# Kernel optimization log

Measured on AMD Instinct MI355X. Metric: run time of the kernel, lower is better.

The kernel has to match this reference:

```python
import jax, jax.numpy as jnp
import numpy as np

NEMB = 128
N_NODES = 8192
N_EDGES = 16384
N_STEMS = 4096
N_GRAPHS = 256
N_BLOCKS = 105       # BlockDictionary.n_unique_blocks
N_STEMTYPES = 32     # BlockDictionary.n_stem_types
OUT_PER_STEM = 105
OUT_PER_STOP = 1
NUM_CONV_STEPS = 12
SLOPE = 0.01         # nn.LeakyReLU default negative slope


def _act(v):
    return jax.nn.leaky_relu(v, SLOPE)


def setup_inputs() -> dict:
    key = jax.random.key(0)
    ks = jax.random.split(key, 32)
    def p(i, shape, fan_in):
        return jax.random.normal(ks[i], shape, jnp.float32) / np.sqrt(fan_in).astype(np.float32)
    D = NEMB
    inp = {
        "x": jax.random.randint(ks[0], (N_NODES,), 0, N_BLOCKS + 1),
        "stemtypes": jax.random.randint(ks[1], (N_STEMS,), 0, N_STEMTYPES + 1),
        "edge_attr": jax.random.randint(ks[2], (N_EDGES, 2), 0, N_STEMTYPES),
        "edge_index": jax.random.randint(ks[3], (2, N_EDGES), 0, N_NODES),
        "stem_node_idx": jax.random.randint(ks[4], (N_STEMS,), 0, N_NODES),
        "node_batch": jnp.sort(jax.random.randint(ks[5], (N_NODES,), 0, N_GRAPHS)),
        # embedding tables
        "emb_block": p(6, (N_BLOCKS + 1, D), D),
        "emb_stem": p(7, (N_STEMTYPES + 1, D), D),
        "emb_bond": p(8, (N_STEMTYPES, D), D),
        # block2emb MLP
        "b2e_w1": p(9, (D, D), D), "b2e_b1": p(10, (D,), D),
        "b2e_w2": p(11, (D, D), D), "b2e_b2": p(12, (D,), D),
        # NNConv root weight + bias (edge-nn is identity: nn.Sequential())
        "conv_root": p(13, (D, D), D), "conv_bias": p(14, (D,), D),
        # GRU (torch gate order r, z, n)
        "gru_w_ih": p(15, (3 * D, D), D), "gru_w_hh": p(16, (3 * D, D), D),
        "gru_b_ih": p(17, (3 * D,), D), "gru_b_hh": p(18, (3 * D,), D),
        # stem2pred MLP (in = 2*D)
        "s2p_w1": p(19, (D, 2 * D), 2 * D), "s2p_b1": p(20, (D,), 2 * D),
        "s2p_w2": p(21, (D, D), D), "s2p_b2": p(22, (D,), D),
        "s2p_w3": p(23, (OUT_PER_STEM, D), D), "s2p_b3": p(24, (OUT_PER_STEM,), D),
        # global2pred MLP
        "g2p_w1": p(25, (D, D), D), "g2p_b1": p(26, (D,), D),
        "g2p_w2": p(27, (OUT_PER_STOP, D), D), "g2p_b2": p(28, (OUT_PER_STOP,), D),
    }
    return inp


def reference(x, stemtypes, edge_attr, edge_index, stem_node_idx, node_batch,
              emb_block, emb_stem, emb_bond,
              b2e_w1, b2e_b1, b2e_w2, b2e_b2,
              conv_root, conv_bias,
              gru_w_ih, gru_w_hh, gru_b_ih, gru_b_hh,
              s2p_w1, s2p_b1, s2p_w2, s2p_b2, s2p_w3, s2p_b3,
              g2p_w1, g2p_b1, g2p_w2, g2p_b2):
    block_emb = emb_block[x]                          # [N, D]
    stem_emb = emb_stem[stemtypes]                    # [S, D]
    be = emb_bond[edge_attr]                          # [E, 2, D]
    # outer product -> per-edge [D_in, D_out] weight (matches view(-1, in, out))
    W_e = be[:, 0, :, None] * be[:, 1, None, :]       # [E, D, D]

    out = _act(block_emb @ b2e_w1.T + b2e_b1) @ b2e_w2.T + b2e_b2  # [N, D]
    h = out                                           # GRU hidden state

    src, dst = edge_index[0], edge_index[1]
    ones_e = jnp.ones((N_EDGES,), out.dtype)
    deg = jax.ops.segment_sum(ones_e, dst, num_segments=N_NODES)
    inv_deg = jnp.where(deg > 0, 1.0 / jnp.maximum(deg, 1.0), 0.0)[:, None]

    for _ in range(NUM_CONV_STEPS):
        # NNConv: mean_j (x_j @ W_e) + x @ root + bias, then LeakyReLU
        msg = jnp.einsum('ei,eij->ej', out[src], W_e)                  # [E, D]
        agg = jax.ops.segment_sum(msg, dst, num_segments=N_NODES) * inv_deg
        m = _act(agg + out @ conv_root + conv_bias)
        # single-layer GRU, seq_len = 1
        gi = m @ gru_w_ih.T + gru_b_ih
        gh = h @ gru_w_hh.T + gru_b_hh
        ir, iz, inn = jnp.split(gi, 3, axis=-1)
        hr, hz, hn = jnp.split(gh, 3, axis=-1)
        r = jax.nn.sigmoid(ir + hr)
        z = jax.nn.sigmoid(iz + hz)
        n = jnp.tanh(inn + r * hn)
        h = (1.0 - z) * n + z * h
        out = h

    stem_cat = jnp.concatenate([out[stem_node_idx], stem_emb], axis=1)  # [S, 2D]
    s = _act(stem_cat @ s2p_w1.T + s2p_b1)
    s = _act(s @ s2p_w2.T + s2p_b2)
    stem_pred = s @ s2p_w3.T + s2p_b3                                   # [S, out_per_stem]

    # global_mean_pool
    gsum = jax.ops.segment_sum(out, node_batch, num_segments=N_GRAPHS)
    gcnt = jax.ops.segment_sum(jnp.ones((N_NODES,), out.dtype), node_batch, num_segments=N_GRAPHS)
    gmean = gsum / jnp.maximum(gcnt, 1.0)[:, None]
    g = _act(gmean @ g2p_w1.T + g2p_b1)
    stop_pred = g @ g2p_w2.T + g2p_b2                                   # [G, out_per_stop]
    return stem_pred, stop_pred
```

## Files before the change

kernel.cpp:

```cpp
#include <hip/hip_runtime.h>
#include <math.h>

#define D 128
#define NNODES 8192
#define NEDGES 16384
#define NSTEMS 4096
#define NGRAPHS 256
#define NSTEPS 12
#define OPS 105
#define SLOPE 0.01f
#define MT 32
#define NB (NNODES / MT)
#define LDA 136
#define LDA2 264
#define LDQ 40
#define LDH 132

typedef _Float16 half_t;
typedef __attribute__((ext_vector_type(8))) _Float16 f16x8;
typedef __attribute__((ext_vector_type(4))) float f32x4;

__device__ __forceinline__ float leaky(float x) { return x > 0.f ? x : SLOPE * x; }
__device__ __forceinline__ float fast_sigmoid(float x) {
    return __builtin_amdgcn_rcpf(1.f + __expf(-x));
}
__device__ __forceinline__ float fast_tanh(float x) {
    float e = __expf(2.f * x);
    return 1.f - 2.f * __builtin_amdgcn_rcpf(e + 1.f);
}

__global__ void k_setup(
    const float* __restrict__ root, const float* __restrict__ wih,
    const float* __restrict__ whh, const float* __restrict__ bond,
    const float* __restrict__ sw1, const float* __restrict__ sw2,
    const float* __restrict__ sw3, const float* __restrict__ bw1,
    const float* __restrict__ bw2, const float* __restrict__ gw1,
    half_t* __restrict__ rootP, half_t* __restrict__ WihP,
    half_t* __restrict__ WhhP, half_t* __restrict__ bondTP,
    half_t* __restrict__ s1P, half_t* __restrict__ s2P, half_t* __restrict__ s3P,
    half_t* __restrict__ w1P, half_t* __restrict__ w2P, half_t* __restrict__ bondQP,
    float* __restrict__ g1T, int* __restrict__ zeroi) {
    int idx = blockIdx.x * 256 + threadIdx.x;
    int which = blockIdx.y;
    if (which == 10) {
        if (idx < 128 * 128) {
            int r = idx >> 7, c = idx & 127;
            g1T[c * 128 + r] = gw1[idx];
        }
        return;
    }
    if (which == 11) {
        if (idx < 2 * NNODES) zeroi[idx] = 0;
        return;
    }
    int KT = (which == 4) ? 8 : (which == 9) ? 1 : 4;
    int NT = (which == 1 || which == 2) ? 24 : (which == 3) ? 2 : (which == 6) ? 7 : 8;
    if (idx >= NT * KT * 512) return;
    int j = idx & 7;
    int L = (idx >> 3) & 63;
    int t = idx >> 9;
    int kt = t % KT, nt = t / KT;
    int k = kt * 32 + (L >> 4) * 8 + j;
    int n = nt * 16 + (L & 15);
    switch (which) {
        case 0: rootP[idx] = (half_t)root[k * D + n]; break;
        case 1: WihP[idx] = (half_t)wih[n * D + k]; break;
        case 2: WhhP[idx] = (half_t)whh[n * D + k]; break;
        case 3: bondTP[idx] = (half_t)bond[n * D + k]; break;
        case 4: s1P[idx] = (half_t)sw1[n * 256 + k]; break;
        case 5: s2P[idx] = (half_t)sw2[n * 128 + k]; break;
        case 6: s3P[idx] = (n < OPS) ? (half_t)sw3[n * 128 + k] : (half_t)0.f; break;
        case 7: w1P[idx] = (half_t)bw1[n * D + k]; break;
        case 8: w2P[idx] = (half_t)bw2[n * D + k]; break;
        case 9: bondQP[idx] = (half_t)bond[k * D + n]; break;
    }
}

__global__ void k_deg(const int* __restrict__ eidx, int* __restrict__ deg) {
    int e = blockIdx.x * 256 + threadIdx.x;
    if (e < NEDGES) atomicAdd(&deg[eidx[NEDGES + e]], 1);
}

__global__ void k_scan(const int* __restrict__ deg, int* __restrict__ row_start,
                       float* __restrict__ inv_deg) {
    __shared__ int sums[256];
    int t = threadIdx.x;
    int base = t * 32;
    int s = 0;
    for (int k = 0; k < 32; ++k) s += deg[base + k];
    sums[t] = s;
    __syncthreads();
    for (int off = 1; off < 256; off <<= 1) {
        int v = sums[t];
        int u = (t >= off) ? sums[t - off] : 0;
        __syncthreads();
        sums[t] = v + u;
        __syncthreads();
    }
    int run = sums[t] - s;
    for (int k = 0; k < 32; ++k) {
        int d = deg[base + k];
        row_start[base + k] = run;
        run += d;
        inv_deg[base + k] = (d > 0) ? (1.0f / (float)d) : 0.0f;
    }
    if (t == 255) row_start[NNODES] = run;
}

__global__ void k_scatter(const int* __restrict__ eidx, const int* __restrict__ eattr,
                          const int* __restrict__ row_start,
                          int* __restrict__ fill, int4* __restrict__ epack) {
    int e = blockIdx.x * 256 + threadIdx.x;
    if (e < NEDGES) {
        int d = eidx[NEDGES + e];
        int pos = row_start[d] + atomicAdd(&fill[d], 1);
        int2 aa = *(const int2*)(eattr + 2 * e);
        epack[pos] = make_int4(eidx[e], aa.x, aa.y, d);
    }
}

__global__ __launch_bounds__(512, 2) void k_init(
    const int* __restrict__ x, const float* __restrict__ embBlock,
    const half_t* __restrict__ w1P, const float* __restrict__ b1,
    const half_t* __restrict__ w2P, const float* __restrict__ b2,
    const half_t* __restrict__ bondTP,
    float* __restrict__ hF, float* __restrict__ P0) {
    __shared__ __align__(16) half_t Ae[MT * LDA];
    __shared__ __align__(16) half_t T1[MT * LDA];
    const int tid = threadIdx.x;
    const int w = tid >> 6;
    const int lane = tid & 63;
    const int quad = lane >> 4;
    const int l16 = lane & 15;
    const int n0 = blockIdx.x * MT;
    const int c = w * 16 + l16;

    {
        int row = tid >> 4;
        int col = (tid & 15) * 8;
        const float* src = embBlock + (size_t)x[n0 + row] * D + col;
        float4 v0 = ((const float4*)src)[0];
        float4 v1 = ((const float4*)src)[1];
        f16x8 hv;
        hv[0] = (half_t)v0.x; hv[1] = (half_t)v0.y; hv[2] = (half_t)v0.z; hv[3] = (half_t)v0.w;
        hv[4] = (half_t)v1.x; hv[5] = (half_t)v1.y; hv[6] = (half_t)v1.z; hv[7] = (half_t)v1.w;
        *(f16x8*)&Ae[row * LDA + col] = hv;
    }
    __syncthreads();

    {
        f32x4 acc[2] = {{0.f, 0.f, 0.f, 0.f}, {0.f, 0.f, 0.f, 0.f}};
#pragma unroll
        for (int kt = 0; kt < 4; ++kt) {
            f16x8 b = *(const f16x8*)(w1P + (size_t)((w * 4 + kt) * 64 + lane) * 8);
            f16x8 a0 = *(const f16x8*)&Ae[(0 + l16) * LDA + kt * 32 + quad * 8];
            f16x8 a1 = *(const f16x8*)&Ae[(16 + l16) * LDA + kt * 32 + quad * 8];
            acc[0] = __builtin_amdgcn_mfma_f32_16x16x32_f16(a0, b, acc[0], 0, 0, 0);
            acc[1] = __builtin_amdgcn_mfma_f32_16x16x32_f16(a1, b, acc[1], 0, 0, 0);
        }
        float bb = b1[c];
#pragma unroll
        for (int mt = 0; mt < 2; ++mt)
#pragma unroll
            for (int r = 0; r < 4; ++r)
                T1[(mt * 16 + quad * 4 + r) * LDA + c] = (half_t)leaky(acc[mt][r] + bb);
    }
    __syncthreads();

    {
        f32x4 acc[2] = {{0.f, 0.f, 0.f, 0.f}, {0.f, 0.f, 0.f, 0.f}};
#pragma unroll
        for (int kt = 0; kt < 4; ++kt) {
            f16x8 b = *(const f16x8*)(w2P + (size_t)((w * 4 + kt) * 64 + lane) * 8);
            f16x8 a0 = *(const f16x8*)&T1[(0 + l16) * LDA + kt * 32 + quad * 8];
            f16x8 a1 = *(const f16x8*)&T1[(16 + l16) * LDA + kt * 32 + quad * 8];
            acc[0] = __builtin_amdgcn_mfma_f32_16x16x32_f16(a0, b, acc[0], 0, 0, 0);
            acc[1] = __builtin_amdgcn_mfma_f32_16x16x32_f16(a1, b, acc[1], 0, 0, 0);
        }
        float bb = b2[c];
#pragma unroll
        for (int mt = 0; mt < 2; ++mt)
#pragma unroll
            for (int r = 0; r < 4; ++r) {
                int row = mt * 16 + quad * 4 + r;
                float h = acc[mt][r] + bb;
                hF[(size_t)(n0 + row) * D + c] = h;
                Ae[row * LDA + c] = (half_t)h;
            }
    }
    __syncthreads();

    if (w < 4) {
        int mt = w >> 1, nt = w & 1;
        f32x4 acc = {0.f, 0.f, 0.f, 0.f};
#pragma unroll
        for (int kt = 0; kt < 4; ++kt) {
            f16x8 b = *(const f16x8*)(bondTP + (size_t)((nt * 4 + kt) * 64 + lane) * 8);
            f16x8 a = *(const f16x8*)&Ae[(mt * 16 + l16) * LDA + kt * 32 + quad * 8];
            acc = __builtin_amdgcn_mfma_f32_16x16x32_f16(a, b, acc, 0, 0, 0);
        }
#pragma unroll
        for (int r = 0; r < 4; ++r)
            P0[(size_t)(n0 + mt * 16 + quad * 4 + r) * 32 + nt * 16 + l16] = acc[r];
    }
}

__global__ __launch_bounds__(512, 2) void k_step(
    float* __restrict__ hF,
    const float* __restrict__ Pprev, float* __restrict__ Pnext,
    const half_t* __restrict__ rootP, const half_t* __restrict__ WihP,
    const half_t* __restrict__ WhhP, const half_t* __restrict__ bondTP,
    const half_t* __restrict__ bondQP,
    const float* __restrict__ cbias, const float* __restrict__ bih,
    const float* __restrict__ bhh,
    const int4* __restrict__ epack,
    const int* __restrict__ row_start, const float* __restrict__ inv_deg, int writeP) {
    __shared__ __align__(16) half_t As[MT * LDA];
    __shared__ __align__(16) half_t Am[MT * LDA];
    __shared__ __align__(16) float Hs[MT * LDH];
    __shared__ __align__(16) half_t Qh[MT * LDQ];
    __shared__ float Q[MT * 32];

    const int tid = threadIdx.x;
    const int w = tid >> 6;
    const int lane = tid & 63;
    const int quad = lane >> 4;
    const int l16 = lane & 15;
    const int n0 = blockIdx.x * MT;
    const int c = w * 16 + l16;

    {
        int row = tid >> 4;
        int col = (tid & 15) * 8;
        const float* src = hF + (size_t)(n0 + row) * D + col;
        float4 v0 = ((const float4*)src)[0];
        float4 v1 = ((const float4*)src)[1];
        f16x8 hv;
        hv[0] = (half_t)v0.x; hv[1] = (half_t)v0.y; hv[2] = (half_t)v0.z; hv[3] = (half_t)v0.w;
        hv[4] = (half_t)v1.x; hv[5] = (half_t)v1.y; hv[6] = (half_t)v1.z; hv[7] = (half_t)v1.w;
        *(f16x8*)&As[row * LDA + col] = hv;
        *(float4*)&Hs[row * LDH + col] = v0;
        *(float4*)&Hs[row * LDH + col + 4] = v1;
    }
    Q[tid] = 0.f;
    Q[tid + 512] = 0.f;
    const int p0 = row_start[n0];
    const int p1 = row_start[n0 + MT];
    int4 ep;
    float wv = 0.f, idg = 0.f;
    const int pme = p0 + tid;
    const bool have = (pme < p1);
    if (have) {
        ep = epack[pme];
        wv = Pprev[(size_t)ep.x * 32 + ep.y];
        idg = inv_deg[ep.w];
    }
    f16x8 rootB[4], ghB[12], aggB;
#pragma unroll
    for (int kt = 0; kt < 4; ++kt)
        rootB[kt] = *(const f16x8*)(rootP + (size_t)((w * 4 + kt) * 64 + lane) * 8);
#pragma unroll
    for (int kt = 0; kt < 4; ++kt)
#pragma unroll
        for (int g = 0; g < 3; ++g)
            ghB[g * 4 + kt] = *(const f16x8*)(WhhP + (size_t)(((g * 8 + w) * 4 + kt) * 64 + lane) * 8);
    aggB = *(const f16x8*)(bondQP + (size_t)(w * 64 + lane) * 8);
    const float cb = cbias[c];
    const float bi0 = bih[c], bi1 = bih[D + c], bi2 = bih[2 * D + c];
    const float bh0 = bhh[c], bh1 = bhh[D + c], bh2 = bhh[2 * D + c];
    __syncthreads();

    f32x4 convAcc[2] = {{0.f, 0.f, 0.f, 0.f}, {0.f, 0.f, 0.f, 0.f}};
#pragma unroll
    for (int kt = 0; kt < 4; ++kt) {
        f16x8 a0 = *(const f16x8*)&As[(0 + l16) * LDA + kt * 32 + quad * 8];
        f16x8 a1 = *(const f16x8*)&As[(16 + l16) * LDA + kt * 32 + quad * 8];
        convAcc[0] = __builtin_amdgcn_mfma_f32_16x16x32_f16(a0, rootB[kt], convAcc[0], 0, 0, 0);
        convAcc[1] = __builtin_amdgcn_mfma_f32_16x16x32_f16(a1, rootB[kt], convAcc[1], 0, 0, 0);
    }
    if (have) atomicAdd(&Q[(ep.w - n0) * 32 + ep.z], wv * idg);
    for (int p2 = pme + 512; p2 < p1; p2 += 512) {
        int4 e2 = epack[p2];
        atomicAdd(&Q[(e2.w - n0) * 32 + e2.z], Pprev[(size_t)e2.x * 32 + e2.y] * inv_deg[e2.w]);
    }
    f32x4 ghA[2][3];
#pragma unroll
    for (int mt = 0; mt < 2; ++mt)
#pragma unroll
        for (int g = 0; g < 3; ++g) ghA[mt][g] = f32x4{0.f, 0.f, 0.f, 0.f};
#pragma unroll
    for (int kt = 0; kt < 4; ++kt) {
        f16x8 a0 = *(const f16x8*)&As[(0 + l16) * LDA + kt * 32 + quad * 8];
        f16x8 a1 = *(const f16x8*)&As[(16 + l16) * LDA + kt * 32 + quad * 8];
#pragma unroll
        for (int g = 0; g < 3; ++g) {
            ghA[0][g] = __builtin_amdgcn_mfma_f32_16x16x32_f16(a0, ghB[g * 4 + kt], ghA[0][g], 0, 0, 0);
            ghA[1][g] = __builtin_amdgcn_mfma_f32_16x16x32_f16(a1, ghB[g * 4 + kt], ghA[1][g], 0, 0, 0);
        }
    }
    __syncthreads();

    f16x8 giB[12];
#pragma unroll
    for (int kt = 0; kt < 4; ++kt)
#pragma unroll
        for (int g = 0; g < 3; ++g)
            giB[g * 4 + kt] = *(const f16x8*)(WihP + (size_t)(((g * 8 + w) * 4 + kt) * 64 + lane) * 8);

    Qh[(tid >> 5) * LDQ + (tid & 31)] = (half_t)Q[tid];
    Qh[((tid + 512) >> 5) * LDQ + (tid & 31)] = (half_t)Q[tid + 512];
    __syncthreads();

#pragma unroll
    for (int mt = 0; mt < 2; ++mt) {
        f32x4 acc = {0.f, 0.f, 0.f, 0.f};
        f16x8 a = *(const f16x8*)&Qh[(mt * 16 + l16) * LDQ + quad * 8];
        acc = __builtin_amdgcn_mfma_f32_16x16x32_f16(a, aggB, acc, 0, 0, 0);
#pragma unroll
        for (int r = 0; r < 4; ++r) {
            float m = convAcc[mt][r] + cb + acc[r];
            Am[(mt * 16 + quad * 4 + r) * LDA + c] = (half_t)leaky(m);
        }
    }
    __syncthreads();

    f32x4 giA[2][3];
#pragma unroll
    for (int mt = 0; mt < 2; ++mt)
#pragma unroll
        for (int g = 0; g < 3; ++g) giA[mt][g] = f32x4{0.f, 0.f, 0.f, 0.f};
#pragma unroll
    for (int kt = 0; kt < 4; ++kt) {
        f16x8 a0 = *(const f16x8*)&Am[(0 + l16) * LDA + kt * 32 + quad * 8];
        f16x8 a1 = *(const f16x8*)&Am[(16 + l16) * LDA + kt * 32 + quad * 8];
#pragma unroll
        for (int g = 0; g < 3; ++g) {
            giA[0][g] = __builtin_amdgcn_mfma_f32_16x16x32_f16(a0, giB[g * 4 + kt], giA[0][g], 0, 0, 0);
            giA[1][g] = __builtin_amdgcn_mfma_f32_16x16x32_f16(a1, giB[g * 4 + kt], giA[1][g], 0, 0, 0);
        }
    }
#pragma unroll
    for (int mt = 0; mt < 2; ++mt) {
#pragma unroll
        for (int r = 0; r < 4; ++r) {
            int row = mt * 16 + quad * 4 + r;
            float rg = fast_sigmoid(giA[mt][0][r] + bi0 + ghA[mt][0][r] + bh0);
            float z = fast_sigmoid(giA[mt][1][r] + bi1 + ghA[mt][1][r] + bh1);
            float nn = fast_tanh(giA[mt][2][r] + bi2 + rg * (ghA[mt][2][r] + bh2));
            float hnew = (1.f - z) * nn + z * Hs[row * LDH + c];
            hF[(size_t)(n0 + row) * D + c] = hnew;
            As[row * LDA + c] = (half_t)hnew;
        }
    }

    if (writeP) {
        __syncthreads();
        if (w < 4) {
            int mt = w >> 1, nt = w & 1;
            f32x4 acc = {0.f, 0.f, 0.f, 0.f};
#pragma unroll
            for (int kt = 0; kt < 4; ++kt) {
                f16x8 b = *(const f16x8*)(bondTP + (size_t)((nt * 4 + kt) * 64 + lane) * 8);
                f16x8 a = *(const f16x8*)&As[(mt * 16 + l16) * LDA + kt * 32 + quad * 8];
                acc = __builtin_amdgcn_mfma_f32_16x16x32_f16(a, b, acc, 0, 0, 0);
            }
#pragma unroll
            for (int r = 0; r < 4; ++r)
                Pnext[(size_t)(n0 + mt * 16 + quad * 4 + r) * 32 + nt * 16 + l16] = acc[r];
        }
    }
}

__device__ __forceinline__ int lower_bound_dev(const int* a, int n, int v) {
    int lo = 0, hi = n;
    while (lo < hi) {
        int m = (lo + hi) >> 1;
        if (a[m] < v) lo = m + 1;
        else hi = m;
    }
    return lo;
}

__global__ __launch_bounds__(512) void k_heads(
    const float* __restrict__ hF, const int* __restrict__ sni, const int* __restrict__ stypes,
    const float* __restrict__ embStem,
    const half_t* __restrict__ s1P, const float* __restrict__ b1,
    const half_t* __restrict__ s2P, const float* __restrict__ b2,
    const half_t* __restrict__ s3P, const float* __restrict__ b3,
    const int* __restrict__ batch,
    const float* __restrict__ g1T, const float* __restrict__ gb1,
    const float* __restrict__ gw2, const float* __restrict__ gb2,
    float* __restrict__ dout) {
    __shared__ __align__(16) half_t cat[16 * LDA2];
    __shared__ __align__(16) half_t t1[16 * LDA];
    __shared__ __align__(16) half_t t2[16 * LDA];
    const int tid = threadIdx.x;
    if (blockIdx.x >= 256) {
        int g = blockIdx.x - 256;
        if (tid >= 128) return;
        __shared__ float mean_s[D];
        __shared__ float red[D];
        int j = tid;
        int lo = lower_bound_dev(batch, NNODES, g);
        int hi = lower_bound_dev(batch, NNODES, g + 1);
        float sum = 0.f;
        for (int n = lo; n < hi; ++n) sum += hF[(size_t)n * D + j];
        float denom = (hi > lo) ? (float)(hi - lo) : 1.0f;
        mean_s[j] = sum / denom;
        __syncthreads();
        float a = gb1[j];
        for (int i = 0; i < D; ++i) a += mean_s[i] * g1T[i * D + j];
        a = leaky(a);
        red[j] = a * gw2[j];
        __syncthreads();
        for (int off = 64; off > 0; off >>= 1) {
            if (j < off) red[j] += red[j + off];
            __syncthreads();
        }
        if (j == 0) dout[NSTEMS * OPS + g] = red[0] + gb2[0];
        return;
    }
    const int w = tid >> 6;
    const int lane = tid & 63;
    const int quad = lane >> 4;
    const int l16 = lane & 15;
    const int s0 = blockIdx.x * 16;
    const int c = w * 16 + l16;

    {
        int row = tid >> 5;
        int col = (tid & 31) * 8;
        const float* src;
        if (col < D) src = hF + (size_t)sni[s0 + row] * D + col;
        else src = embStem + (size_t)stypes[s0 + row] * D + (col - D);
        float4 v0 = ((const float4*)src)[0];
        float4 v1 = ((const float4*)src)[1];
        f16x8 hv;
        hv[0] = (half_t)v0.x; hv[1] = (half_t)v0.y; hv[2] = (half_t)v0.z; hv[3] = (half_t)v0.w;
        hv[4] = (half_t)v1.x; hv[5] = (half_t)v1.y; hv[6] = (half_t)v1.z; hv[7] = (half_t)v1.w;
        *(f16x8*)&cat[row * LDA2 + col] = hv;
    }
    __syncthreads();

    {
        f32x4 acc = {0.f, 0.f, 0.f, 0.f};
#pragma unroll
        for (int kt = 0; kt < 8; ++kt) {
            f16x8 b = *(const f16x8*)(s1P + (size_t)((w * 8 + kt) * 64 + lane) * 8);
            f16x8 a = *(const f16x8*)&cat[l16 * LDA2 + kt * 32 + quad * 8];
            acc = __builtin_amdgcn_mfma_f32_16x16x32_f16(a, b, acc, 0, 0, 0);
        }
        float bb = b1[c];
#pragma unroll
        for (int r = 0; r < 4; ++r)
            t1[(quad * 4 + r) * LDA + c] = (half_t)leaky(acc[r] + bb);
    }
    __syncthreads();
    {
        f32x4 acc = {0.f, 0.f, 0.f, 0.f};
#pragma unroll
        for (int kt = 0; kt < 4; ++kt) {
            f16x8 b = *(const f16x8*)(s2P + (size_t)((w * 4 + kt) * 64 + lane) * 8);
            f16x8 a = *(const f16x8*)&t1[l16 * LDA + kt * 32 + quad * 8];
            acc = __builtin_amdgcn_mfma_f32_16x16x32_f16(a, b, acc, 0, 0, 0);
        }
        float bb = b2[c];
#pragma unroll
        for (int r = 0; r < 4; ++r)
            t2[(quad * 4 + r) * LDA + c] = (half_t)leaky(acc[r] + bb);
    }
    __syncthreads();
    if (w < 7) {
        f32x4 acc = {0.f, 0.f, 0.f, 0.f};
#pragma unroll
        for (int kt = 0; kt < 4; ++kt) {
            f16x8 b = *(const f16x8*)(s3P + (size_t)((w * 4 + kt) * 64 + lane) * 8);
            f16x8 a = *(const f16x8*)&t2[l16 * LDA + kt * 32 + quad * 8];
            acc = __builtin_amdgcn_mfma_f32_16x16x32_f16(a, b, acc, 0, 0, 0);
        }
        int j = w * 16 + l16;
        if (j < OPS) {
            float bb = b3[j];
#pragma unroll
            for (int r = 0; r < 4; ++r)
                dout[(size_t)(s0 + quad * 4 + r) * OPS + j] = acc[r] + bb;
        }
    }
}

extern "C" void kernel_launch(void* const* d_in, const int* in_sizes, int n_in,
                              void* d_out, int out_size, void* d_ws, size_t ws_size,
                              hipStream_t stream) {
    const int* x = (const int*)d_in[0];
    const int* stypes = (const int*)d_in[1];
    const int* eattr = (const int*)d_in[2];
    const int* eidx = (const int*)d_in[3];
    const int* sni = (const int*)d_in[4];
    const int* batch = (const int*)d_in[5];
    const float* embBlock = (const float*)d_in[6];
    const float* embStem = (const float*)d_in[7];
    const float* embBond = (const float*)d_in[8];
    const float* b2e_w1 = (const float*)d_in[9];
    const float* b2e_b1 = (const float*)d_in[10];
    const float* b2e_w2 = (const float*)d_in[11];
    const float* b2e_b2 = (const float*)d_in[12];
    const float* conv_root = (const float*)d_in[13];
    const float* conv_bias = (const float*)d_in[14];
    const float* gru_w_ih = (const float*)d_in[15];
    const float* gru_w_hh = (const float*)d_in[16];
    const float* gru_b_ih = (const float*)d_in[17];
    const float* gru_b_hh = (const float*)d_in[18];
    const float* s2p_w1 = (const float*)d_in[19];
    const float* s2p_b1 = (const float*)d_in[20];
    const float* s2p_w2 = (const float*)d_in[21];
    const float* s2p_b2 = (const float*)d_in[22];
    const float* s2p_w3 = (const float*)d_in[23];
    const float* s2p_b3 = (const float*)d_in[24];
    const float* g2p_w1 = (const float*)d_in[25];
    const float* g2p_b1 = (const float*)d_in[26];
    const float* g2p_w2 = (const float*)d_in[27];
    const float* g2p_b2 = (const float*)d_in[28];
    float* out_f = (float*)d_out;

    float* W = (float*)d_ws;
    size_t off = 0;
    auto alloc = [&](size_t words) {
        size_t o = off;
        off += (words + 3) & ~(size_t)3;
        return o;
    };
    float* hF = W + alloc(NNODES * D);
    float* P0 = W + alloc(NNODES * 32);
    float* P1 = W + alloc(NNODES * 32);
    half_t* rootP = (half_t*)(W + alloc(16384 / 2));
    half_t* WihP = (half_t*)(W + alloc(49152 / 2));
    half_t* WhhP = (half_t*)(W + alloc(49152 / 2));
    half_t* bondTP = (half_t*)(W + alloc(4096 / 2));
    half_t* s1P = (half_t*)(W + alloc(32768 / 2));
    half_t* s2P = (half_t*)(W + alloc(16384 / 2));
    half_t* s3P = (half_t*)(W + alloc(14336 / 2));
    half_t* w1P = (half_t*)(W + alloc(16384 / 2));
    half_t* w2P = (half_t*)(W + alloc(16384 / 2));
    half_t* bondQP = (half_t*)(W + alloc(4096 / 2));
    float* g1T = W + alloc(128 * 128);
    int* row_start = (int*)(W + alloc(NNODES + 1));
    int4* epack = (int4*)(W + alloc(NEDGES * 4));
    float* inv_deg = W + alloc(NNODES);
    float* zbase = W + alloc(2 * NNODES);
    int* deg = (int*)zbase;
    int* fill = deg + NNODES;

    k_setup<<<dim3(192, 12), 256, 0, stream>>>(
        conv_root, gru_w_ih, gru_w_hh, embBond, s2p_w1, s2p_w2, s2p_w3,
        b2e_w1, b2e_w2, g2p_w1,
        rootP, WihP, WhhP, bondTP, s1P, s2P, s3P, w1P, w2P, bondQP,
        g1T, (int*)zbase);
    k_deg<<<(NEDGES + 255) / 256, 256, 0, stream>>>(eidx, deg);
    k_scan<<<1, 256, 0, stream>>>(deg, row_start, inv_deg);
    k_scatter<<<(NEDGES + 255) / 256, 256, 0, stream>>>(eidx, eattr, row_start, fill, epack);
    k_init<<<NNODES / MT, 512, 0, stream>>>(x, embBlock, w1P, b2e_b1, w2P, b2e_b2,
                                            bondTP, hF, P0);

    for (int step = 0; step < NSTEPS; ++step) {
        const float* Pprev = (step & 1) ? P1 : P0;
        float* Pnext = (step & 1) ? P0 : P1;
        int writeP = (step < NSTEPS - 1) ? 1 : 0;
        k_step<<<NB, 512, 0, stream>>>(
            hF, Pprev, Pnext, rootP, WihP, WhhP, bondTP, bondQP,
            conv_bias, gru_b_ih, gru_b_hh,
            epack, row_start, inv_deg, writeP);
    }

    k_heads<<<NSTEMS / 16 + NGRAPHS, 512, 0, stream>>>(
        hF, sni, stypes, embStem,
        s1P, s2p_b1, s2P, s2p_b2, s3P, s2p_b3,
        batch, g1T, g2p_b1, g2p_w2, g2p_b2, out_f);
}
```

Measured before the change: 251.7 us.

## Halve step-kernel node tile to 16 rows for more blocks and occupancy

Each k_step block now processes 16 nodes instead of 32, doubling the grid to 512 blocks so more of the GPU's compute units are busy. Weight fragments for the GRU matrices are loaded inside the MFMA loops instead of being preloaded into registers, and launch bounds are raised to allow four blocks per CU. The trade-off is that each block rereads the same weights for half as many rows, and each wave does less MFMA work per weight load.

```diff
diff --git a/kernel.cpp b/kernel.cpp
--- a/kernel.cpp
+++ b/kernel.cpp
@@ -9,8 +9,9 @@
 #define NSTEPS 12
 #define OPS 105
 #define SLOPE 0.01f
-#define MT 32
-#define NB (NNODES / MT)
+#define IMT 32
+#define MTS 16
+#define NBS (NNODES / MTS)
 #define LDA 136
 #define LDA2 264
 #define LDQ 40
@@ -125,14 +126,14 @@
     const half_t* __restrict__ w2P, const float* __restrict__ b2,
     const half_t* __restrict__ bondTP,
     float* __restrict__ hF, float* __restrict__ P0) {
-    __shared__ __align__(16) half_t Ae[MT * LDA];
-    __shared__ __align__(16) half_t T1[MT * LDA];
+    __shared__ __align__(16) half_t Ae[IMT * LDA];
+    __shared__ __align__(16) half_t T1[IMT * LDA];
     const int tid = threadIdx.x;
     const int w = tid >> 6;
     const int lane = tid & 63;
     const int quad = lane >> 4;
     const int l16 = lane & 15;
-    const int n0 = blockIdx.x * MT;
+    const int n0 = blockIdx.x * IMT;
     const int c = w * 16 + l16;
 
     {
@@ -205,7 +206,7 @@
     }
 }
 
-__global__ __launch_bounds__(512, 2) void k_step(
+__global__ __launch_bounds__(512, 4) void k_step(
     float* __restrict__ hF,
     const float* __restrict__ Pprev, float* __restrict__ Pnext,
     const half_t* __restrict__ rootP, const half_t* __restrict__ WihP,
@@ -215,37 +216,31 @@
     const float* __restrict__ bhh,
     const int4* __restrict__ epack,
     const int* __restrict__ row_start, const float* __restrict__ inv_deg, int writeP) {
-    __shared__ __align__(16) half_t As[MT * LDA];
-    __shared__ __align__(16) half_t Am[MT * LDA];
-    __shared__ __align__(16) float Hs[MT * LDH];
-    __shared__ __align__(16) half_t Qh[MT * LDQ];
-    __shared__ float Q[MT * 32];
+    __shared__ __align__(16) half_t As[MTS * LDA];
+    __shared__ __align__(16) half_t Am[MTS * LDA];
+    __shared__ __align__(16) float Hs[MTS * LDH];
+    __shared__ __align__(16) half_t Qh[MTS * LDQ];
+    __shared__ float Q[MTS * 32];
 
     const int tid = threadIdx.x;
     const int w = tid >> 6;
     const int lane = tid & 63;
     const int quad = lane >> 4;
     const int l16 = lane & 15;
-    const int n0 = blockIdx.x * MT;
+    const int n0 = blockIdx.x * MTS;
     const int c = w * 16 + l16;
 
     {
-        int row = tid >> 4;
-        int col = (tid & 15) * 8;
-        const float* src = hF + (size_t)(n0 + row) * D + col;
-        float4 v0 = ((const float4*)src)[0];
-        float4 v1 = ((const float4*)src)[1];
-        f16x8 hv;
-        hv[0] = (half_t)v0.x; hv[1] = (half_t)v0.y; hv[2] = (half_t)v0.z; hv[3] = (half_t)v0.w;
-        hv[4] = (half_t)v1.x; hv[5] = (half_t)v1.y; hv[6] = (half_t)v1.z; hv[7] = (half_t)v1.w;
-        *(f16x8*)&As[row * LDA + col] = hv;
-        *(float4*)&Hs[row * LDH + col] = v0;
-        *(float4*)&Hs[row * LDH + col + 4] = v1;
-    }
-    Q[tid] = 0.f;
-    Q[tid + 512] = 0.f;
+        int row = tid >> 5;
+        int col = (tid & 31) * 4;
+        float4 v = *(const float4*)(hF + (size_t)(n0 + row) * D + col);
+        half_t* dst = &As[row * LDA + col];
+        dst[0] = (half_t)v.x; dst[1] = (half_t)v.y; dst[2] = (half_t)v.z; dst[3] = (half_t)v.w;
+        *(float4*)&Hs[row * LDH + col] = v;
+    }
+    if (tid < MTS * 32) Q[tid] = 0.f;
     const int p0 = row_start[n0];
-    const int p1 = row_start[n0 + MT];
+    const int p1 = row_start[n0 + MTS];
     int4 ep;
     float wv = 0.f, idg = 0.f;
     const int pme = p0 + tid;
@@ -255,118 +250,88 @@
         wv = Pprev[(size_t)ep.x * 32 + ep.y];
         idg = inv_deg[ep.w];
     }
-    f16x8 rootB[4], ghB[12], aggB;
+    f16x8 rootB[4];
 #pragma unroll
     for (int kt = 0; kt < 4; ++kt)
         rootB[kt] = *(const f16x8*)(rootP + (size_t)((w * 4 + kt) * 64 + lane) * 8);
-#pragma unroll
-    for (int kt = 0; kt < 4; ++kt)
-#pragma unroll
-        for (int g = 0; g < 3; ++g)
-            ghB[g * 4 + kt] = *(const f16x8*)(WhhP + (size_t)(((g * 8 + w) * 4 + kt) * 64 + lane) * 8);
-    aggB = *(const f16x8*)(bondQP + (size_t)(w * 64 + lane) * 8);
+    f16x8 aggB = *(const f16x8*)(bondQP + (size_t)(w * 64 + lane) * 8);
     const float cb = cbias[c];
     const float bi0 = bih[c], bi1 = bih[D + c], bi2 = bih[2 * D + c];
     const float bh0 = bhh[c], bh1 = bhh[D + c], bh2 = bhh[2 * D + c];
     __syncthreads();
 
-    f32x4 convAcc[2] = {{0.f, 0.f, 0.f, 0.f}, {0.f, 0.f, 0.f, 0.f}};
+    f32x4 convAcc = {0.f, 0.f, 0.f, 0.f};
 #pragma unroll
     for (int kt = 0; kt < 4; ++kt) {
-        f16x8 a0 = *(const f16x8*)&As[(0 + l16) * LDA + kt * 32 + quad * 8];
-        f16x8 a1 = *(const f16x8*)&As[(16 + l16) * LDA + kt * 32 + quad * 8];
-        convAcc[0] = __builtin_amdgcn_mfma_f32_16x16x32_f16(a0, rootB[kt], convAcc[0], 0, 0, 0);
-        convAcc[1] = __builtin_amdgcn_mfma_f32_16x16x32_f16(a1, rootB[kt], convAcc[1], 0, 0, 0);
+        f16x8 a = *(const f16x8*)&As[l16 * LDA + kt * 32 + quad * 8];
+        convAcc = __builtin_amdgcn_mfma_f32_16x16x32_f16(a, rootB[kt], convAcc, 0, 0, 0);
     }
     if (have) atomicAdd(&Q[(ep.w - n0) * 32 + ep.z], wv * idg);
     for (int p2 = pme + 512; p2 < p1; p2 += 512) {
         int4 e2 = epack[p2];
         atomicAdd(&Q[(e2.w - n0) * 32 + e2.z], Pprev[(size_t)e2.x * 32 + e2.y] * inv_deg[e2.w]);
     }
-    f32x4 ghA[2][3];
-#pragma unroll
-    for (int mt = 0; mt < 2; ++mt)
-#pragma unroll
-        for (int g = 0; g < 3; ++g) ghA[mt][g] = f32x4{0.f, 0.f, 0.f, 0.f};
+    f32x4 ghA[3] = {{0.f, 0.f, 0.f, 0.f}, {0.f, 0.f, 0.f, 0.f}, {0.f, 0.f, 0.f, 0.f}};
 #pragma unroll
     for (int kt = 0; kt < 4; ++kt) {
-        f16x8 a0 = *(const f16x8*)&As[(0 + l16) * LDA + kt * 32 + quad * 8];
-        f16x8 a1 = *(const f16x8*)&As[(16 + l16) * LDA + kt * 32 + quad * 8];
+        f16x8 a = *(const f16x8*)&As[l16 * LDA + kt * 32 + quad * 8];
 #pragma unroll
         for (int g = 0; g < 3; ++g) {
-            ghA[0][g] = __builtin_amdgcn_mfma_f32_16x16x32_f16(a0, ghB[g * 4 + kt], ghA[0][g], 0, 0, 0);
-            ghA[1][g] = __builtin_amdgcn_mfma_f32_16x16x32_f16(a1, ghB[g * 4 + kt], ghA[1][g], 0, 0, 0);
-        }
-    }
-    __syncthreads();
-
-    f16x8 giB[12];
-#pragma unroll
-    for (int kt = 0; kt < 4; ++kt)
-#pragma unroll
-        for (int g = 0; g < 3; ++g)
-            giB[g * 4 + kt] = *(const f16x8*)(WihP + (size_t)(((g * 8 + w) * 4 + kt) * 64 + lane) * 8);
-
-    Qh[(tid >> 5) * LDQ + (tid & 31)] = (half_t)Q[tid];
-    Qh[((tid + 512) >> 5) * LDQ + (tid & 31)] = (half_t)Q[tid + 512];
-    __syncthreads();
-
-#pragma unroll
-    for (int mt = 0; mt < 2; ++mt) {
+            f16x8 b = *(const f16x8*)(WhhP + (size_t)(((g * 8 + w) * 4 + kt) * 64 + lane) * 8);
+            ghA[g] = __builtin_amdgcn_mfma_f32_16x16x32_f16(a, b, ghA[g], 0, 0, 0);
+        }
+    }
+    __syncthreads();
+
+    if (tid < MTS * 32) Qh[(tid >> 5) * LDQ + (tid & 31)] = (half_t)Q[tid];
+    __syncthreads();
+
+    {
         f32x4 acc = {0.f, 0.f, 0.f, 0.f};
-        f16x8 a = *(const f16x8*)&Qh[(mt * 16 + l16) * LDQ + quad * 8];
+        f16x8 a = *(const f16x8*)&Qh[l16 * LDQ + quad * 8];
         acc = __builtin_amdgcn_mfma_f32_16x16x32_f16(a, aggB, acc, 0, 0, 0);
 #pragma unroll
         for (int r = 0; r < 4; ++r) {
-            float m = convAcc[mt][r] + cb + acc[r];
-            Am[(mt * 16 + quad * 4 + r) * LDA + c] = (half_t)leaky(m);
-        }
-    }
-    __syncthreads();
-
-    f32x4 giA[2][3];
-#pragma unroll
-    for (int mt = 0; mt < 2; ++mt)
-#pragma unroll
-        for (int g = 0; g < 3; ++g) giA[mt][g] = f32x4{0.f, 0.f, 0.f, 0.f};
+            float m = convAcc[r] + cb + acc[r];
+            Am[(quad * 4 + r) * LDA + c] = (half_t)leaky(m);
+        }
+    }
+    __syncthreads();
+
+    f32x4 giA[3] = {{0.f, 0.f, 0.f, 0.f}, {0.f, 0.f, 0.f, 0.f}, {0.f, 0.f, 0.f, 0.f}};
 #pragma unroll
     for (int kt = 0; kt < 4; ++kt) {
-        f16x8 a0 = *(const f16x8*)&Am[(0 + l16) * LDA + kt * 32 + quad * 8];
-        f16x8 a1 = *(const f16x8*)&Am[(16 + l16) * LDA + kt * 32 + quad * 8];
+        f16x8 a = *(const f16x8*)&Am[l16 * LDA + kt * 32 + quad * 8];
 #pragma unroll
         for (int g = 0; g < 3; ++g) {
-            giA[0][g] = __builtin_amdgcn_mfma_f32_16x16x32_f16(a0, giB[g * 4 + kt], giA[0][g], 0, 0, 0);
-            giA[1][g] = __builtin_amdgcn_mfma_f32_16x16x32_f16(a1, giB[g * 4 + kt], giA[1][g], 0, 0, 0);
-        }
-    }
-#pragma unroll
-    for (int mt = 0; mt < 2; ++mt) {
-#pragma unroll
-        for (int r = 0; r < 4; ++r) {
-            int row = mt * 16 + quad * 4 + r;
-            float rg = fast_sigmoid(giA[mt][0][r] + bi0 + ghA[mt][0][r] + bh0);
-            float z = fast_sigmoid(giA[mt][1][r] + bi1 + ghA[mt][1][r] + bh1);
-            float nn = fast_tanh(giA[mt][2][r] + bi2 + rg * (ghA[mt][2][r] + bh2));
-            float hnew = (1.f - z) * nn + z * Hs[row * LDH + c];
-            hF[(size_t)(n0 + row) * D + c] = hnew;
-            As[row * LDA + c] = (half_t)hnew;
-        }
+            f16x8 b = *(const f16x8*)(WihP + (size_t)(((g * 8 + w) * 4 + kt) * 64 + lane) * 8);
+            giA[g] = __builtin_amdgcn_mfma_f32_16x16x32_f16(a, b, giA[g], 0, 0, 0);
+        }
+    }
+#pragma unroll
+    for (int r = 0; r < 4; ++r) {
+        int row = quad * 4 + r;
+        float rg = fast_sigmoid(giA[0][r] + bi0 + ghA[0][r] + bh0);
+        float z = fast_sigmoid(giA[1][r] + bi1 + ghA[1][r] + bh1);
+        float nn = fast_tanh(giA[2][r] + bi2 + rg * (ghA[2][r] + bh2));
+        float hnew = (1.f - z) * nn + z * Hs[row * LDH + c];
+        hF[(size_t)(n0 + row) * D + c] = hnew;
+        As[row * LDA + c] = (half_t)hnew;
     }
 
     if (writeP) {
         __syncthreads();
-        if (w < 4) {
-            int mt = w >> 1, nt = w & 1;
+        if (w < 2) {
             f32x4 acc = {0.f, 0.f, 0.f, 0.f};
 #pragma unroll
             for (int kt = 0; kt < 4; ++kt) {
-                f16x8 b = *(const f16x8*)(bondTP + (size_t)((nt * 4 + kt) * 64 + lane) * 8);
-                f16x8 a = *(const f16x8*)&As[(mt * 16 + l16) * LDA + kt * 32 + quad * 8];
+                f16x8 b = *(const f16x8*)(bondTP + (size_t)((w * 4 + kt) * 64 + lane) * 8);
+                f16x8 a = *(const f16x8*)&As[l16 * LDA + kt * 32 + quad * 8];
                 acc = __builtin_amdgcn_mfma_f32_16x16x32_f16(a, b, acc, 0, 0, 0);
             }
 #pragma unroll
             for (int r = 0; r < 4; ++r)
-                Pnext[(size_t)(n0 + mt * 16 + quad * 4 + r) * 32 + nt * 16 + l16] = acc[r];
+                Pnext[(size_t)(n0 + quad * 4 + r) * 32 + w * 16 + l16] = acc[r];
         }
     }
 }
@@ -558,14 +523,14 @@
     k_deg<<<(NEDGES + 255) / 256, 256, 0, stream>>>(eidx, deg);
     k_scan<<<1, 256, 0, stream>>>(deg, row_start, inv_deg);
     k_scatter<<<(NEDGES + 255) / 256, 256, 0, stream>>>(eidx, eattr, row_start, fill, epack);
-    k_init<<<NNODES / MT, 512, 0, stream>>>(x, embBlock, w1P, b2e_b1, w2P, b2e_b2,
-                                            bondTP, hF, P0);
+    k_init<<<NNODES / IMT, 512, 0, stream>>>(x, embBlock, w1P, b2e_b1, w2P, b2e_b2,
+                                             bondTP, hF, P0);
 
     for (int step = 0; step < NSTEPS; ++step) {
         const float* Pprev = (step & 1) ? P1 : P0;
         float* Pnext = (step & 1) ? P0 : P1;
         int writeP = (step < NSTEPS - 1) ? 1 : 0;
-        k_step<<<NB, 512, 0, stream>>>(
+        k_step<<<NBS, 512, 0, stream>>>(
             hF, Pprev, Pnext, rootP, WihP, WhhP, bondTP, bondQP,
             conv_bias, gru_b_ih, gru_b_hh,
             epack, row_start, inv_deg, writeP);
```

Result: slower. 271.5 us (+7.9%).

## Fuse all GRU message-passing steps into one persistent kernel with grid barriers

Applied to the files above, without the earlier changes.

Replaces the twelve per-step kernel launches with a single persistent kernel of 256 blocks that loops over steps and uses a global atomic counter barrier between steps. Hidden state stays in registers across steps instead of round-tripping through global memory, weights are loaded once, and inv_deg scaling moves from per-edge to per-row. It removes launch overhead and repeated weight/state loads, at the cost of relying on all blocks being co-resident (deadlock risk otherwise) and spin-wait barrier latency.

```diff
diff --git a/kernel.cpp b/kernel.cpp
--- a/kernel.cpp
+++ b/kernel.cpp
@@ -10,11 +10,10 @@
 #define OPS 105
 #define SLOPE 0.01f
 #define MT 32
-#define NB (NNODES / MT)
+#define NBLK (NNODES / MT)
 #define LDA 136
 #define LDA2 264
 #define LDQ 40
-#define LDH 132
 
 typedef _Float16 half_t;
 typedef __attribute__((ext_vector_type(8))) _Float16 f16x8;
@@ -50,7 +49,7 @@
         return;
     }
     if (which == 11) {
-        if (idx < 2 * NNODES) zeroi[idx] = 0;
+        if (idx < 2 * NNODES + 64) zeroi[idx] = 0;
         return;
     }
     int KT = (which == 4) ? 8 : (which == 9) ? 1 : 4;
@@ -205,19 +204,19 @@
     }
 }
 
-__global__ __launch_bounds__(512, 2) void k_step(
+__global__ __launch_bounds__(512, 2) void k_mega(
     float* __restrict__ hF,
-    const float* __restrict__ Pprev, float* __restrict__ Pnext,
+    float* __restrict__ P0, float* __restrict__ P1,
     const half_t* __restrict__ rootP, const half_t* __restrict__ WihP,
     const half_t* __restrict__ WhhP, const half_t* __restrict__ bondTP,
     const half_t* __restrict__ bondQP,
     const float* __restrict__ cbias, const float* __restrict__ bih,
     const float* __restrict__ bhh,
     const int4* __restrict__ epack,
-    const int* __restrict__ row_start, const float* __restrict__ inv_deg, int writeP) {
+    const int* __restrict__ row_start, const float* __restrict__ inv_deg,
+    int* __restrict__ ctr) {
     __shared__ __align__(16) half_t As[MT * LDA];
     __shared__ __align__(16) half_t Am[MT * LDA];
-    __shared__ __align__(16) float Hs[MT * LDH];
     __shared__ __align__(16) half_t Qh[MT * LDQ];
     __shared__ float Q[MT * 32];
 
@@ -229,146 +228,153 @@
     const int n0 = blockIdx.x * MT;
     const int c = w * 16 + l16;
 
-    {
-        int row = tid >> 4;
-        int col = (tid & 15) * 8;
-        const float* src = hF + (size_t)(n0 + row) * D + col;
-        float4 v0 = ((const float4*)src)[0];
-        float4 v1 = ((const float4*)src)[1];
-        f16x8 hv;
-        hv[0] = (half_t)v0.x; hv[1] = (half_t)v0.y; hv[2] = (half_t)v0.z; hv[3] = (half_t)v0.w;
-        hv[4] = (half_t)v1.x; hv[5] = (half_t)v1.y; hv[6] = (half_t)v1.z; hv[7] = (half_t)v1.w;
-        *(f16x8*)&As[row * LDA + col] = hv;
-        *(float4*)&Hs[row * LDH + col] = v0;
-        *(float4*)&Hs[row * LDH + col + 4] = v1;
-    }
+    f16x8 rootB[4], ghB[12], giB[12], aggB;
+#pragma unroll
+    for (int kt = 0; kt < 4; ++kt)
+        rootB[kt] = *(const f16x8*)(rootP + (size_t)((w * 4 + kt) * 64 + lane) * 8);
+#pragma unroll
+    for (int kt = 0; kt < 4; ++kt)
+#pragma unroll
+        for (int g = 0; g < 3; ++g) {
+            ghB[g * 4 + kt] = *(const f16x8*)(WhhP + (size_t)(((g * 8 + w) * 4 + kt) * 64 + lane) * 8);
+            giB[g * 4 + kt] = *(const f16x8*)(WihP + (size_t)(((g * 8 + w) * 4 + kt) * 64 + lane) * 8);
+        }
+    aggB = *(const f16x8*)(bondQP + (size_t)(w * 64 + lane) * 8);
+
+    float h[2][4];
+#pragma unroll
+    for (int mt = 0; mt < 2; ++mt)
+#pragma unroll
+        for (int r = 0; r < 4; ++r) {
+            int row = mt * 16 + quad * 4 + r;
+            float v = hF[(size_t)(n0 + row) * D + c];
+            h[mt][r] = v;
+            As[row * LDA + c] = (half_t)v;
+        }
     Q[tid] = 0.f;
     Q[tid + 512] = 0.f;
     const int p0 = row_start[n0];
     const int p1 = row_start[n0 + MT];
-    int4 ep;
-    float wv = 0.f, idg = 0.f;
-    const int pme = p0 + tid;
-    const bool have = (pme < p1);
-    if (have) {
-        ep = epack[pme];
-        wv = Pprev[(size_t)ep.x * 32 + ep.y];
-        idg = inv_deg[ep.w];
-    }
-    f16x8 rootB[4], ghB[12], aggB;
-#pragma unroll
-    for (int kt = 0; kt < 4; ++kt)
-        rootB[kt] = *(const f16x8*)(rootP + (size_t)((w * 4 + kt) * 64 + lane) * 8);
-#pragma unroll
-    for (int kt = 0; kt < 4; ++kt)
-#pragma unroll
-        for (int g = 0; g < 3; ++g)
-            ghB[g * 4 + kt] = *(const f16x8*)(WhhP + (size_t)(((g * 8 + w) * 4 + kt) * 64 + lane) * 8);
-    aggB = *(const f16x8*)(bondQP + (size_t)(w * 64 + lane) * 8);
     const float cb = cbias[c];
     const float bi0 = bih[c], bi1 = bih[D + c], bi2 = bih[2 * D + c];
     const float bh0 = bhh[c], bh1 = bhh[D + c], bh2 = bhh[2 * D + c];
-    __syncthreads();
-
-    f32x4 convAcc[2] = {{0.f, 0.f, 0.f, 0.f}, {0.f, 0.f, 0.f, 0.f}};
-#pragma unroll
-    for (int kt = 0; kt < 4; ++kt) {
-        f16x8 a0 = *(const f16x8*)&As[(0 + l16) * LDA + kt * 32 + quad * 8];
-        f16x8 a1 = *(const f16x8*)&As[(16 + l16) * LDA + kt * 32 + quad * 8];
-        convAcc[0] = __builtin_amdgcn_mfma_f32_16x16x32_f16(a0, rootB[kt], convAcc[0], 0, 0, 0);
-        convAcc[1] = __builtin_amdgcn_mfma_f32_16x16x32_f16(a1, rootB[kt], convAcc[1], 0, 0, 0);
-    }
-    if (have) atomicAdd(&Q[(ep.w - n0) * 32 + ep.z], wv * idg);
-    for (int p2 = pme + 512; p2 < p1; p2 += 512) {
-        int4 e2 = epack[p2];
-        atomicAdd(&Q[(e2.w - n0) * 32 + e2.z], Pprev[(size_t)e2.x * 32 + e2.y] * inv_deg[e2.w]);
-    }
-    f32x4 ghA[2][3];
+    const int qrow0 = tid >> 5, qrow1 = (tid + 512) >> 5;
+    const float idg0 = inv_deg[n0 + qrow0];
+    const float idg1 = inv_deg[n0 + qrow1];
+    __syncthreads();
+
+    for (int s = 0; s < NSTEPS; ++s) {
+        const float* __restrict__ Pprev = (s & 1) ? P1 : P0;
+        float* __restrict__ Pnext = (s & 1) ? P0 : P1;
+
+        for (int p = p0 + tid; p < p1; p += 512) {
+            int4 ep = epack[p];
+            float wv = __hip_atomic_load(&Pprev[(size_t)ep.x * 32 + ep.y],
+                                         __ATOMIC_RELAXED, __HIP_MEMORY_SCOPE_AGENT);
+            atomicAdd(&Q[(ep.w - n0) * 32 + ep.z], wv);
+        }
+
+        f32x4 convAcc[2] = {{0.f, 0.f, 0.f, 0.f}, {0.f, 0.f, 0.f, 0.f}};
+        f32x4 ghA[2][3];
+#pragma unroll
+        for (int mt = 0; mt < 2; ++mt)
+#pragma unroll
+            for (int g = 0; g < 3; ++g) ghA[mt][g] = f32x4{0.f, 0.f, 0.f, 0.f};
+#pragma unroll
+        for (int kt = 0; kt < 4; ++kt) {
+            f16x8 a0 = *(const f16x8*)&As[(0 + l16) * LDA + kt * 32 + quad * 8];
+            f16x8 a1 = *(const f16x8*)&As[(16 + l16) * LDA + kt * 32 + quad * 8];
+            convAcc[0] = __builtin_amdgcn_mfma_f32_16x16x32_f16(a0, rootB[kt], convAcc[0], 0, 0, 0);
+            convAcc[1] = __builtin_amdgcn_mfma_f32_16x16x32_f16(a1, rootB[kt], convAcc[1], 0, 0, 0);
+#pragma unroll
+            for (int g = 0; g < 3; ++g) {
+                ghA[0][g] = __builtin_amdgcn_mfma_f32_16x16x32_f16(a0, ghB[g * 4 + kt], ghA[0][g], 0, 0, 0);
+                ghA[1][g] = __builtin_amdgcn_mfma_f32_16x16x32_f16(a1, ghB[g * 4 + kt], ghA[1][g], 0, 0, 0);
+            }
+        }
+        __syncthreads();
+
+        Qh[qrow0 * LDQ + (tid & 31)] = (half_t)(Q[tid] * idg0);
+        Qh[qrow1 * LDQ + (tid & 31)] = (half_t)(Q[tid + 512] * idg1);
+        Q[tid] = 0.f;
+        Q[tid + 512] = 0.f;
+        __syncthreads();
+
+#pragma unroll
+        for (int mt = 0; mt < 2; ++mt) {
+            f32x4 acc = {0.f, 0.f, 0.f, 0.f};
+            f16x8 a = *(const f16x8*)&Qh[(mt * 16 + l16) * LDQ + quad * 8];
+            acc = __builtin_amdgcn_mfma_f32_16x16x32_f16(a, aggB, acc, 0, 0, 0);
+#pragma unroll
+            for (int r = 0; r < 4; ++r) {
+                float m = convAcc[mt][r] + cb + acc[r];
+                Am[(mt * 16 + quad * 4 + r) * LDA + c] = (half_t)leaky(m);
+            }
+        }
+        __syncthreads();
+
+        f32x4 giA[2][3];
+#pragma unroll
+        for (int mt = 0; mt < 2; ++mt)
+#pragma unroll
+            for (int g = 0; g < 3; ++g) giA[mt][g] = f32x4{0.f, 0.f, 0.f, 0.f};
+#pragma unroll
+        for (int kt = 0; kt < 4; ++kt) {
+            f16x8 a0 = *(const f16x8*)&Am[(0 + l16) * LDA + kt * 32 + quad * 8];
+            f16x8 a1 = *(const f16x8*)&Am[(16 + l16) * LDA + kt * 32 + quad * 8];
+#pragma unroll
+            for (int g = 0; g < 3; ++g) {
+                giA[0][g] = __builtin_amdgcn_mfma_f32_16x16x32_f16(a0, giB[g * 4 + kt], giA[0][g], 0, 0, 0);
+                giA[1][g] = __builtin_amdgcn_mfma_f32_16x16x32_f16(a1, giB[g * 4 + kt], giA[1][g], 0, 0, 0);
+            }
+        }
+#pragma unroll
+        for (int mt = 0; mt < 2; ++mt) {
+#pragma unroll
+            for (int r = 0; r < 4; ++r) {
+                int row = mt * 16 + quad * 4 + r;
+                float rg = fast_sigmoid(giA[mt][0][r] + bi0 + ghA[mt][0][r] + bh0);
+                float z = fast_sigmoid(giA[mt][1][r] + bi1 + ghA[mt][1][r] + bh1);
+                float nn = fast_tanh(giA[mt][2][r] + bi2 + rg * (ghA[mt][2][r] + bh2));
+                float hnew = (1.f - z) * nn + z * h[mt][r];
+                h[mt][r] = hnew;
+                As[row * LDA + c] = (half_t)hnew;
+            }
+        }
+
+        if (s < NSTEPS - 1) {
+            __syncthreads();
+            if (w < 4) {
+                int mt = w >> 1, nt = w & 1;
+                f32x4 acc = {0.f, 0.f, 0.f, 0.f};
+#pragma unroll
+                for (int kt = 0; kt < 4; ++kt) {
+                    f16x8 b = *(const f16x8*)(bondTP + (size_t)((nt * 4 + kt) * 64 + lane) * 8);
+                    f16x8 a = *(const f16x8*)&As[(mt * 16 + l16) * LDA + kt * 32 + quad * 8];
+                    acc = __builtin_amdgcn_mfma_f32_16x16x32_f16(a, b, acc, 0, 0, 0);
+                }
+#pragma unroll
+                for (int r = 0; r < 4; ++r)
+                    __hip_atomic_store(&Pnext[(size_t)(n0 + mt * 16 + quad * 4 + r) * 32 + nt * 16 + l16],
+                                       acc[r], __ATOMIC_RELAXED, __HIP_MEMORY_SCOPE_AGENT);
+            }
+            __syncthreads();
+            if (tid == 0) {
+                __hip_atomic_fetch_add(&ctr[s], 1, __ATOMIC_RELEASE, __HIP_MEMORY_SCOPE_AGENT);
+                while (__hip_atomic_load(&ctr[s], __ATOMIC_RELAXED, __HIP_MEMORY_SCOPE_AGENT) < NBLK)
+                    __builtin_amdgcn_s_sleep(1);
+            }
+            __syncthreads();
+        }
+    }
+
 #pragma unroll
     for (int mt = 0; mt < 2; ++mt)
-#pragma unroll
-        for (int g = 0; g < 3; ++g) ghA[mt][g] = f32x4{0.f, 0.f, 0.f, 0.f};
-#pragma unroll
-    for (int kt = 0; kt < 4; ++kt) {
-        f16x8 a0 = *(const f16x8*)&As[(0 + l16) * LDA + kt * 32 + quad * 8];
-        f16x8 a1 = *(const f16x8*)&As[(16 + l16) * LDA + kt * 32 + quad * 8];
-#pragma unroll
-        for (int g = 0; g < 3; ++g) {
-            ghA[0][g] = __builtin_amdgcn_mfma_f32_16x16x32_f16(a0, ghB[g * 4 + kt], ghA[0][g], 0, 0, 0);
-            ghA[1][g] = __builtin_amdgcn_mfma_f32_16x16x32_f16(a1, ghB[g * 4 + kt], ghA[1][g], 0, 0, 0);
-        }
-    }
-    __syncthreads();
-
-    f16x8 giB[12];
-#pragma unroll
-    for (int kt = 0; kt < 4; ++kt)
-#pragma unroll
-        for (int g = 0; g < 3; ++g)
-            giB[g * 4 + kt] = *(const f16x8*)(WihP + (size_t)(((g * 8 + w) * 4 + kt) * 64 + lane) * 8);
-
-    Qh[(tid >> 5) * LDQ + (tid & 31)] = (half_t)Q[tid];
-    Qh[((tid + 512) >> 5) * LDQ + (tid & 31)] = (half_t)Q[tid + 512];
-    __syncthreads();
-
-#pragma unroll
-    for (int mt = 0; mt < 2; ++mt) {
-        f32x4 acc = {0.f, 0.f, 0.f, 0.f};
-        f16x8 a = *(const f16x8*)&Qh[(mt * 16 + l16) * LDQ + quad * 8];
-        acc = __builtin_amdgcn_mfma_f32_16x16x32_f16(a, aggB, acc, 0, 0, 0);
-#pragma unroll
-        for (int r = 0; r < 4; ++r) {
-            float m = convAcc[mt][r] + cb + acc[r];
-            Am[(mt * 16 + quad * 4 + r) * LDA + c] = (half_t)leaky(m);
-        }
-    }
-    __syncthreads();
-
-    f32x4 giA[2][3];
-#pragma unroll
-    for (int mt = 0; mt < 2; ++mt)
-#pragma unroll
-        for (int g = 0; g < 3; ++g) giA[mt][g] = f32x4{0.f, 0.f, 0.f, 0.f};
-#pragma unroll
-    for (int kt = 0; kt < 4; ++kt) {
-        f16x8 a0 = *(const f16x8*)&Am[(0 + l16) * LDA + kt * 32 + quad * 8];
-        f16x8 a1 = *(const f16x8*)&Am[(16 + l16) * LDA + kt * 32 + quad * 8];
-#pragma unroll
-        for (int g = 0; g < 3; ++g) {
-            giA[0][g] = __builtin_amdgcn_mfma_f32_16x16x32_f16(a0, giB[g * 4 + kt], giA[0][g], 0, 0, 0);
-            giA[1][g] = __builtin_amdgcn_mfma_f32_16x16x32_f16(a1, giB[g * 4 + kt], giA[1][g], 0, 0, 0);
-        }
-    }
-#pragma unroll
-    for (int mt = 0; mt < 2; ++mt) {
 #pragma unroll
         for (int r = 0; r < 4; ++r) {
             int row = mt * 16 + quad * 4 + r;
-            float rg = fast_sigmoid(giA[mt][0][r] + bi0 + ghA[mt][0][r] + bh0);
-            float z = fast_sigmoid(giA[mt][1][r] + bi1 + ghA[mt][1][r] + bh1);
-            float nn = fast_tanh(giA[mt][2][r] + bi2 + rg * (ghA[mt][2][r] + bh2));
-            float hnew = (1.f - z) * nn + z * Hs[row * LDH + c];
-            hF[(size_t)(n0 + row) * D + c] = hnew;
-            As[row * LDA + c] = (half_t)hnew;
-        }
-    }
-
-    if (writeP) {
-        __syncthreads();
-        if (w < 4) {
-            int mt = w >> 1, nt = w & 1;
-            f32x4 acc = {0.f, 0.f, 0.f, 0.f};
-#pragma unroll
-            for (int kt = 0; kt < 4; ++kt) {
-                f16x8 b = *(const f16x8*)(bondTP + (size_t)((nt * 4 + kt) * 64 + lane) * 8);
-                f16x8 a = *(const f16x8*)&As[(mt * 16 + l16) * LDA + kt * 32 + quad * 8];
-                acc = __builtin_amdgcn_mfma_f32_16x16x32_f16(a, b, acc, 0, 0, 0);
-            }
-#pragma unroll
-            for (int r = 0; r < 4; ++r)
-                Pnext[(size_t)(n0 + mt * 16 + quad * 4 + r) * 32 + nt * 16 + l16] = acc[r];
-        }
-    }
+            hF[(size_t)(n0 + row) * D + c] = h[mt][r];
+        }
 }
 
 __device__ __forceinline__ int lower_bound_dev(const int* a, int n, int v) {
@@ -546,9 +552,10 @@
     int* row_start = (int*)(W + alloc(NNODES + 1));
     int4* epack = (int4*)(W + alloc(NEDGES * 4));
     float* inv_deg = W + alloc(NNODES);
-    float* zbase = W + alloc(2 * NNODES);
+    float* zbase = W + alloc(2 * NNODES + 64);
     int* deg = (int*)zbase;
     int* fill = deg + NNODES;
+    int* ctr = fill + NNODES;
 
     k_setup<<<dim3(192, 12), 256, 0, stream>>>(
         conv_root, gru_w_ih, gru_w_hh, embBond, s2p_w1, s2p_w2, s2p_w3,
@@ -561,15 +568,10 @@
     k_init<<<NNODES / MT, 512, 0, stream>>>(x, embBlock, w1P, b2e_b1, w2P, b2e_b2,
                                             bondTP, hF, P0);
 
-    for (int step = 0; step < NSTEPS; ++step) {
-        const float* Pprev = (step & 1) ? P1 : P0;
-        float* Pnext = (step & 1) ? P0 : P1;
-        int writeP = (step < NSTEPS - 1) ? 1 : 0;
-        k_step<<<NB, 512, 0, stream>>>(
-            hF, Pprev, Pnext, rootP, WihP, WhhP, bondTP, bondQP,
-            conv_bias, gru_b_ih, gru_b_hh,
-            epack, row_start, inv_deg, writeP);
-    }
+    k_mega<<<NBLK, 512, 0, stream>>>(
+        hF, P0, P1, rootP, WihP, WhhP, bondTP, bondQP,
+        conv_bias, gru_b_ih, gru_b_hh,
+        epack, row_start, inv_deg, ctr);
 
     k_heads<<<NSTEMS / 16 + NGRAPHS, 512, 0, stream>>>(
         hF, sni, stypes, embStem,
```

Result: slower. 286.9 us (+14.0%).
